# Kernel tuning notes

Hardware: AMD Instinct MI355X
Metric: run time of the kernel (lower is better)

## Reference

```python
import jax, jax.numpy as jnp
import numpy as np

B, V, D = 8, 201, 256          # batch episodes, nodes (way*shot+1), feature dim
H = 128                        # hidden_dim
CHANS = [D, 2 * H, 2 * H, H, H]  # channel widths per ratio [2,2,1,1]
K = int(0.5 * V)               # beta * V = 100
EPS = 1e-5
SLOPE = 0.01                   # LeakyReLU default negative slope


def setup_inputs() -> dict:
    key = jax.random.key(0)
    ks = jax.random.split(key, 24)
    inp = {"x": jax.random.normal(ks[0], (B, V, D), dtype=jnp.float32)}
    j = 1
    for i in range(4):  # conv + BN blocks
        cin, cout = CHANS[i], CHANS[i + 1]
        inp[f"w{i}"] = jax.random.normal(ks[j], (cout, cin), dtype=jnp.float32) * (1.0 / np.sqrt(cin)); j += 1
        inp[f"b{i}"] = jax.random.normal(ks[j], (cout,), dtype=jnp.float32) * 0.02; j += 1
        inp[f"g{i}"] = 1.0 + 0.1 * jax.random.normal(ks[j], (cout,), dtype=jnp.float32); j += 1
        inp[f"be{i}"] = 0.1 * jax.random.normal(ks[j], (cout,), dtype=jnp.float32); j += 1
    inp["w4"] = jax.random.normal(ks[j], (1, CHANS[-1]), dtype=jnp.float32) * (1.0 / np.sqrt(CHANS[-1])); j += 1
    inp["b4"] = jax.random.normal(ks[j], (1,), dtype=jnp.float32) * 0.02
    return inp


def _bn(a, g, be):
    # BatchNorm2d training-mode forward: batch stats over (B, V, V) per channel
    m = a.mean(axis=(0, 1, 2))
    v = a.var(axis=(0, 1, 2))
    return (a - m) / jnp.sqrt(v + EPS) * g + be


def _block(a, w, b, g, be):
    # 1x1 conv == per-pixel GEMM in channel dim; layout [B,V,V,C]
    a = jnp.einsum("bvwc,oc->bvwo", a, w) + b
    a = _bn(a, g, be)
    return jnp.where(a >= 0, a, SLOPE * a)  # LeakyReLU


def reference(x, w0, b0, g0, be0, w1, b1, g1, be1, w2, b2, g2, be2,
              w3, b3, g3, be3, w4, b4):
    # pairwise abs-diff: [B, V, V, D]
    a = jnp.abs(x[:, :, None, :] - x[:, None, :, :])
    a = _block(a, w0, b0, g0, be0)
    a = _block(a, w1, b1, g1, be1)
    a = _block(a, w2, b2, g2, be2)
    a = _block(a, w3, b3, g3, be3)
    a = jnp.einsum("bvwc,oc->bvwo", a, w4) + b4   # [B, V, V, 1]
    A = jax.nn.softmax(a[..., 0], axis=2)         # softmax over second V axis
    # topk scatter mask, fully vectorized over batch and rows
    vals, idx = jax.lax.top_k(A, K)               # [B, V, K]
    bi = jnp.arange(B)[:, None, None]
    vi = jnp.arange(V)[None, :, None]
    mask_A = jnp.zeros_like(A).at[bi, vi, idx].set(vals)
    return mask_A
```

## Files before the change

### kernel.cpp

```cpp
#include <hip/hip_runtime.h>
#include <math.h>

#define NB 8
#define NV 201
#define ND 256
#define NPIX (NB*NV*NV)
#define TRI  (NV*(NV+1)/2)
#define NSYM (NB*TRI)
#define KSEL 100
#define BN_EPS 1e-5f
#define SLOPE 0.01f

__device__ __forceinline__ float lrelu(float v) { return v >= 0.f ? v : SLOPE * v; }

typedef _Float16 half4_t __attribute__((ext_vector_type(4)));
typedef _Float16 half8   __attribute__((ext_vector_type(8)));
typedef float    f32x4   __attribute__((ext_vector_type(4)));

__device__ __forceinline__ half4_t to_h4(float4 v) {
    half4_t h;
    h.x = (_Float16)v.x; h.y = (_Float16)v.y;
    h.z = (_Float16)v.z; h.w = (_Float16)v.w;
    return h;
}
__device__ __forceinline__ half4_t residual_h4(float4 v, half4_t h) {
    half4_t l;
    l.x = (_Float16)(v.x - (float)h.x); l.y = (_Float16)(v.y - (float)h.y);
    l.z = (_Float16)(v.z - (float)h.z); l.w = (_Float16)(v.w - (float)h.w);
    return l;
}
__device__ __forceinline__ half8 cat8(half4_t a, half4_t b) {
    half8 r;
    r[0] = a.x; r[1] = a.y; r[2] = a.z; r[3] = a.w;
    r[4] = b.x; r[5] = b.y; r[6] = b.z; r[7] = b.w;
    return r;
}

__device__ __forceinline__ int tri_base(int i) { return i * NV - (i * (i - 1)) / 2; }
__device__ __forceinline__ void tri_decode(int s, int& b, int& i, int& j) {
    b = s / TRI;
    int t = s - b * TRI;
    float disc = (float)(403 * 403) - 8.0f * (float)t;
    int ii = (int)((403.0f - sqrtf(disc)) * 0.5f);
    if (ii < 0) ii = 0;
    if (ii > NV - 1) ii = NV - 1;
    while (ii < NV - 1 && tri_base(ii + 1) <= t) ++ii;
    while (ii > 0 && tri_base(ii) > t) --ii;
    i = ii;
    j = t - tri_base(ii) + ii;
}

__device__ __forceinline__ float4 ld4(const float* p) { return *(const float4*)p; }

__global__ void zero_stats(double* p) { p[blockIdx.x * 256 + threadIdx.x] = 0.0; }

template<int CIN, int COUT, int MODE>
__global__ __launch_bounds__(256)
void gemm_bn_mfma(const float* xin,
                  const float* in,
                  const float* __restrict__ W,
                  const float* __restrict__ scale,
                  const float* __restrict__ shift,
                  float* out,
                  double* __restrict__ stat_sum,
                  double* __restrict__ stat_sq)
{
    constexpr int BM  = 128;
    constexpr int BK  = 32;
    constexpr int PAD = 40;
    constexpr int NCW = COUT / 32;
    __shared__ __align__(16) _Float16 Bh[COUT][PAD];
    __shared__ __align__(16) _Float16 Bl[COUT][PAD];
    __shared__ float wg[BM];
    __shared__ int   rbi[(MODE == 0) ? BM : 1];
    __shared__ int   rbj[(MODE == 0) ? BM : 1];

    const int t    = threadIdx.x;
    const int lane = t & 63;
    const int wv   = t >> 6;
    const int wm   = wv >> 1;
    const int wn   = wv & 1;
    const int l15  = lane & 15;
    const int lk   = lane >> 4;
    const int m0   = blockIdx.x * BM;

    for (int m = t; m < BM; m += 256) {
        int pix = m0 + m;
        int b, i, j;
        if (pix < NSYM) {
            tri_decode(pix, b, i, j);
            wg[m] = (i == j) ? 1.f : 2.f;
            if constexpr (MODE == 0) { rbi[m] = b * NV + i; rbj[m] = b * NV + j; }
        } else {
            wg[m] = 0.f;
            if constexpr (MODE == 0) { rbi[m] = 0; rbj[m] = 0; }
        }
    }

    f32x4 acc[4][NCW];
    #pragma unroll
    for (int rt = 0; rt < 4; ++rt)
        #pragma unroll
        for (int nc = 0; nc < NCW; ++nc) {
            acc[rt][nc][0] = 0.f; acc[rt][nc][1] = 0.f;
            acc[rt][nc][2] = 0.f; acc[rt][nc][3] = 0.f;
        }

    for (int kt = 0; kt < CIN; kt += BK) {
        #pragma unroll
        for (int f = 0; f < COUT / 32; ++f) {
            int flat = t + 256 * f;
            int n    = flat >> 3;
            int kq   = flat & 7;
            int k    = kt + kq * 4;
            float4 w = *(const float4*)(W + (size_t)n * CIN + k);
            half4_t vh = to_h4(w);
            half4_t vl = residual_h4(w, vh);
            *(half4_t*)&Bh[n][kq * 4] = vh;
            *(half4_t*)&Bl[n][kq * 4] = vl;
        }
        __syncthreads();

        float4 sc0, sc1, sh0, sh1;
        if constexpr (MODE == 1) {
            sc0 = ld4(scale + kt + lk * 8); sc1 = ld4(scale + kt + lk * 8 + 4);
            sh0 = ld4(shift + kt + lk * 8); sh1 = ld4(shift + kt + lk * 8 + 4);
        }
        half8 ah[4], alo[4];
        #pragma unroll
        for (int rt = 0; rt < 4; ++rt) {
            int m   = wm * 64 + rt * 16 + l15;
            int pix = m0 + m;
            float4 v0 = make_float4(0.f, 0.f, 0.f, 0.f);
            float4 v1 = v0;
            if (pix < NSYM) {
                if constexpr (MODE == 0) {
                    const float* pi = xin + (size_t)rbi[m] * ND + kt + lk * 8;
                    const float* pj = xin + (size_t)rbj[m] * ND + kt + lk * 8;
                    float4 xi0 = ld4(pi), xi1 = ld4(pi + 4);
                    float4 xj0 = ld4(pj), xj1 = ld4(pj + 4);
                    v0 = make_float4(fabsf(xi0.x - xj0.x), fabsf(xi0.y - xj0.y),
                                     fabsf(xi0.z - xj0.z), fabsf(xi0.w - xj0.w));
                    v1 = make_float4(fabsf(xi1.x - xj1.x), fabsf(xi1.y - xj1.y),
                                     fabsf(xi1.z - xj1.z), fabsf(xi1.w - xj1.w));
                } else {
                    const float* p = in + (size_t)pix * 256 + kt + lk * 8;
                    float4 u0 = ld4(p), u1 = ld4(p + 4);
                    v0.x = lrelu(fmaf(u0.x, sc0.x, sh0.x));
                    v0.y = lrelu(fmaf(u0.y, sc0.y, sh0.y));
                    v0.z = lrelu(fmaf(u0.z, sc0.z, sh0.z));
                    v0.w = lrelu(fmaf(u0.w, sc0.w, sh0.w));
                    v1.x = lrelu(fmaf(u1.x, sc1.x, sh1.x));
                    v1.y = lrelu(fmaf(u1.y, sc1.y, sh1.y));
                    v1.z = lrelu(fmaf(u1.z, sc1.z, sh1.z));
                    v1.w = lrelu(fmaf(u1.w, sc1.w, sh1.w));
                }
            }
            half4_t h0 = to_h4(v0), h1 = to_h4(v1);
            half4_t l0 = residual_h4(v0, h0), l1 = residual_h4(v1, h1);
            ah[rt]  = cat8(h0, h1);
            alo[rt] = cat8(l0, l1);
        }

        #pragma unroll
        for (int nc = 0; nc < NCW; ++nc) {
            int ctrow = (wn * NCW + nc) * 16 + l15;
            half8 bh = *(const half8*)&Bh[ctrow][lk * 8];
            half8 bl = *(const half8*)&Bl[ctrow][lk * 8];
            #pragma unroll
            for (int rt = 0; rt < 4; ++rt) {
                acc[rt][nc] = __builtin_amdgcn_mfma_f32_16x16x32_f16(ah[rt],  bh, acc[rt][nc], 0, 0, 0);
                acc[rt][nc] = __builtin_amdgcn_mfma_f32_16x16x32_f16(ah[rt],  bl, acc[rt][nc], 0, 0, 0);
                acc[rt][nc] = __builtin_amdgcn_mfma_f32_16x16x32_f16(alo[rt], bh, acc[rt][nc], 0, 0, 0);
            }
        }
        __syncthreads();
    }

    float* csum = (float*)&Bh[0][0];
    float* csq  = csum + COUT;
    for (int n = t; n < COUT; n += 256) { csum[n] = 0.f; csq[n] = 0.f; }
    __syncthreads();

    float tsum[NCW], tsq[NCW];
    #pragma unroll
    for (int nc = 0; nc < NCW; ++nc) { tsum[nc] = 0.f; tsq[nc] = 0.f; }

    #pragma unroll
    for (int rt = 0; rt < 4; ++rt) {
        #pragma unroll
        for (int r = 0; r < 4; ++r) {
            int row = wm * 64 + rt * 16 + lk * 4 + r;
            int pix = m0 + row;
            if (pix < NSYM) {
                float wgt = wg[row];
                #pragma unroll
                for (int nc = 0; nc < NCW; ++nc) {
                    float v = acc[rt][nc][r];
                    tsum[nc] += wgt * v;
                    tsq[nc]  += wgt * v * v;
                    out[(size_t)pix * 256 + wn * (COUT / 2) + nc * 16 + l15] = v;
                }
            }
        }
    }
    #pragma unroll
    for (int nc = 0; nc < NCW; ++nc) {
        int col = wn * (COUT / 2) + nc * 16 + l15;
        atomicAdd(&csum[col], tsum[nc]);
        atomicAdd(&csq[col],  tsq[nc]);
    }
    __syncthreads();
    for (int n = t; n < COUT; n += 256) {
        atomicAdd(&stat_sum[n], (double)csum[n]);
        atomicAdd(&stat_sq[n],  (double)csq[n]);
    }
}

__global__ void bn_finalize(const double* __restrict__ ssum, const double* __restrict__ ssq,
                            const float* __restrict__ g, const float* __restrict__ be,
                            float* __restrict__ scale, float* __restrict__ shift, int C)
{
    int c = threadIdx.x + blockIdx.x * blockDim.x;
    if (c < C) {
        double m = ssum[c] * (1.0 / NPIX);
        double v = ssq[c] * (1.0 / NPIX) - m * m;
        float s = g[c] / sqrtf((float)v + BN_EPS);
        scale[c] = s;
        shift[c] = be[c] - (float)m * s;
    }
}

__global__ __launch_bounds__(256)
void logits_tri(const float* __restrict__ act,
                const float* __restrict__ scale, const float* __restrict__ shift,
                const float* __restrict__ w4, const float* __restrict__ b4,
                float* __restrict__ lt)
{
    int s = blockIdx.x * 256 + threadIdx.x;
    if (s >= NSYM) return;
    const float* p = act + (size_t)s * 256;
    float acc = 0.f;
    #pragma unroll
    for (int c = 0; c < 128; c += 4) {
        float4 u  = ld4(p + c);
        float4 sc = *(const float4*)(scale + c);
        float4 sh = *(const float4*)(shift + c);
        float4 w  = *(const float4*)(w4 + c);
        acc += lrelu(fmaf(u.x, sc.x, sh.x)) * w.x;
        acc += lrelu(fmaf(u.y, sc.y, sh.y)) * w.y;
        acc += lrelu(fmaf(u.z, sc.z, sh.z)) * w.z;
        acc += lrelu(fmaf(u.w, sc.w, sh.w)) * w.w;
    }
    lt[s] = acc + b4[0];
}

__global__ __launch_bounds__(256)
void final_softmax_topk_sym(const float* __restrict__ lt, float* __restrict__ outp)
{
    __shared__ float sv[NV];
    __shared__ float red[256];
    const int row = blockIdx.x;
    const int b   = row / NV;
    const int i   = row - b * NV;
    const int t   = threadIdx.x;

    float logit = -INFINITY;
    if (t < NV) {
        int jm = (i < t) ? i : t;
        int jM = (i < t) ? t : i;
        logit = lt[b * TRI + tri_base(jm) + (jM - jm)];
    }
    red[t] = logit;
    __syncthreads();
    #pragma unroll
    for (int off = 128; off > 0; off >>= 1) {
        if (t < off) red[t] = fmaxf(red[t], red[t + off]);
        __syncthreads();
    }
    float mx = red[0];
    __syncthreads();
    float e = (t < NV) ? expf(logit - mx) : 0.f;
    red[t] = e;
    __syncthreads();
    #pragma unroll
    for (int off = 128; off > 0; off >>= 1) {
        if (t < off) red[t] += red[t + off];
        __syncthreads();
    }
    float denom = red[0];
    __syncthreads();
    float val = e / denom;
    if (t < NV) sv[t] = val;
    __syncthreads();
    if (t < NV) {
        int rank = 0;
        for (int j = 0; j < NV; ++j) {
            float o = sv[j];
            rank += (o > val || (o == val && j < t)) ? 1 : 0;
        }
        outp[(size_t)row * NV + t] = (rank < KSEL) ? val : 0.f;
    }
}

extern "C" void kernel_launch(void* const* d_in, const int* in_sizes, int n_in,
                              void* d_out, int out_size, void* d_ws, size_t ws_size,
                              hipStream_t stream)
{
    (void)in_sizes; (void)n_in; (void)out_size; (void)ws_size;

    const float* x   = (const float*)d_in[0];
    const float* w0  = (const float*)d_in[1];
    const float* g0  = (const float*)d_in[3];
    const float* be0 = (const float*)d_in[4];
    const float* w1  = (const float*)d_in[5];
    const float* g1  = (const float*)d_in[7];
    const float* be1 = (const float*)d_in[8];
    const float* w2  = (const float*)d_in[9];
    const float* g2  = (const float*)d_in[11];
    const float* be2 = (const float*)d_in[12];
    const float* w3  = (const float*)d_in[13];
    const float* g3  = (const float*)d_in[15];
    const float* be3 = (const float*)d_in[16];
    const float* w4  = (const float*)d_in[17];
    const float* b4  = (const float*)d_in[18];

    char* ws = (char*)d_ws;
    double* D    = (double*)ws;
    float*  F    = (float*)(ws + 16384);
    float*  lt   = (float*)(ws + 16384 + 8192);
    float*  buf  = (float*)(ws + 16384 + 8192 + 655360);
    float*  outp = (float*)d_out;

    zero_stats<<<8, 256, 0, stream>>>(D);

    const int g128 = (NSYM + 127) / 128;

    gemm_bn_mfma<256, 256, 0><<<g128, 256, 0, stream>>>(
        x, nullptr, w0, nullptr, nullptr, buf, D + 0, D + 256);
    bn_finalize<<<1, 256, 0, stream>>>(D + 0, D + 256, g0, be0, F + 0, F + 256, 256);

    gemm_bn_mfma<256, 256, 1><<<g128, 256, 0, stream>>>(
        nullptr, buf, w1, F + 0, F + 256, buf, D + 512, D + 768);
    bn_finalize<<<1, 256, 0, stream>>>(D + 512, D + 768, g1, be1, F + 512, F + 768, 256);

    gemm_bn_mfma<256, 128, 1><<<g128, 256, 0, stream>>>(
        nullptr, buf, w2, F + 512, F + 768, buf, D + 1024, D + 1280);
    bn_finalize<<<1, 256, 0, stream>>>(D + 1024, D + 1280, g2, be2, F + 1024, F + 1280, 128);

    gemm_bn_mfma<128, 128, 1><<<g128, 256, 0, stream>>>(
        nullptr, buf, w3, F + 1024, F + 1280, buf, D + 1536, D + 1792);
    bn_finalize<<<1, 256, 0, stream>>>(D + 1536, D + 1792, g3, be3, F + 1536, F + 1792, 128);

    logits_tri<<<(NSYM + 255) / 256, 256, 0, stream>>>(buf, F + 1536, F + 1792, w4, b4, lt);
    final_softmax_topk_sym<<<NB * NV, 256, 0, stream>>>(lt, outp);
}
```

Measured before the change: 664.9 us.

## Pre-split weights to fp16 hi/lo once and read B fragments directly from global

Adds a one-time kernel that splits all four conv weight matrices into fp16 high and low residual parts, stored in the output buffer as scratch. The GEMM kernels then load B fragments straight from global or L2 instead of converting and staging weights through shared memory every K-tile. This removes the per-tile conversion work and two barriers per K iteration. In exchange, each wave now issues uncoalesced-ish global loads for weights, and the output buffer is reused as temporary storage before the final kernel overwrites it.

```diff
diff --git a/kernel.cpp b/kernel.cpp
--- a/kernel.cpp
+++ b/kernel.cpp
@@ -10,6 +10,7 @@
 #define KSEL 100
 #define BN_EPS 1e-5f
 #define SLOPE 0.01f
+#define NWTOT 180224
 
 __device__ __forceinline__ float lrelu(float v) { return v >= 0.f ? v : SLOPE * v; }
 
@@ -54,11 +55,28 @@
 
 __global__ void zero_stats(double* p) { p[blockIdx.x * 256 + threadIdx.x] = 0.0; }
 
+__global__ void split_weights(const float* __restrict__ w0, const float* __restrict__ w1,
+                              const float* __restrict__ w2, const float* __restrict__ w3,
+                              _Float16* __restrict__ H, _Float16* __restrict__ L)
+{
+    int idx = blockIdx.x * 256 + threadIdx.x;
+    if (idx >= NWTOT) return;
+    float v;
+    if      (idx <  65536) v = w0[idx];
+    else if (idx < 131072) v = w1[idx -  65536];
+    else if (idx < 163840) v = w2[idx - 131072];
+    else                   v = w3[idx - 163840];
+    _Float16 h = (_Float16)v;
+    H[idx] = h;
+    L[idx] = (_Float16)(v - (float)h);
+}
+
 template<int CIN, int COUT, int MODE>
 __global__ __launch_bounds__(256)
 void gemm_bn_mfma(const float* xin,
                   const float* in,
-                  const float* __restrict__ W,
+                  const _Float16* __restrict__ Wh,
+                  const _Float16* __restrict__ Wl,
                   const float* __restrict__ scale,
                   const float* __restrict__ shift,
                   float* out,
@@ -67,13 +85,12 @@
 {
     constexpr int BM  = 128;
     constexpr int BK  = 32;
-    constexpr int PAD = 40;
     constexpr int NCW = COUT / 32;
-    __shared__ __align__(16) _Float16 Bh[COUT][PAD];
-    __shared__ __align__(16) _Float16 Bl[COUT][PAD];
     __shared__ float wg[BM];
     __shared__ int   rbi[(MODE == 0) ? BM : 1];
     __shared__ int   rbj[(MODE == 0) ? BM : 1];
+    __shared__ float csum[COUT];
+    __shared__ float csq[COUT];
 
     const int t    = threadIdx.x;
     const int lane = t & 63;
@@ -96,6 +113,7 @@
             if constexpr (MODE == 0) { rbi[m] = 0; rbj[m] = 0; }
         }
     }
+    __syncthreads();
 
     f32x4 acc[4][NCW];
     #pragma unroll
@@ -107,20 +125,6 @@
         }
 
     for (int kt = 0; kt < CIN; kt += BK) {
-        #pragma unroll
-        for (int f = 0; f < COUT / 32; ++f) {
-            int flat = t + 256 * f;
-            int n    = flat >> 3;
-            int kq   = flat & 7;
-            int k    = kt + kq * 4;
-            float4 w = *(const float4*)(W + (size_t)n * CIN + k);
-            half4_t vh = to_h4(w);
-            half4_t vl = residual_h4(w, vh);
-            *(half4_t*)&Bh[n][kq * 4] = vh;
-            *(half4_t*)&Bl[n][kq * 4] = vl;
-        }
-        __syncthreads();
-
         float4 sc0, sc1, sh0, sh1;
         if constexpr (MODE == 1) {
             sc0 = ld4(scale + kt + lk * 8); sc1 = ld4(scale + kt + lk * 8 + 4);
@@ -164,9 +168,9 @@
 
         #pragma unroll
         for (int nc = 0; nc < NCW; ++nc) {
-            int ctrow = (wn * NCW + nc) * 16 + l15;
-            half8 bh = *(const half8*)&Bh[ctrow][lk * 8];
-            half8 bl = *(const half8*)&Bl[ctrow][lk * 8];
+            size_t boff = (size_t)(wn * (COUT / 2) + nc * 16 + l15) * CIN + kt + lk * 8;
+            half8 bh = *(const half8*)(Wh + boff);
+            half8 bl = *(const half8*)(Wl + boff);
             #pragma unroll
             for (int rt = 0; rt < 4; ++rt) {
                 acc[rt][nc] = __builtin_amdgcn_mfma_f32_16x16x32_f16(ah[rt],  bh, acc[rt][nc], 0, 0, 0);
@@ -174,11 +178,8 @@
                 acc[rt][nc] = __builtin_amdgcn_mfma_f32_16x16x32_f16(alo[rt], bh, acc[rt][nc], 0, 0, 0);
             }
         }
-        __syncthreads();
-    }
-
-    float* csum = (float*)&Bh[0][0];
-    float* csq  = csum + COUT;
+    }
+
     for (int n = t; n < COUT; n += 256) { csum[n] = 0.f; csq[n] = 0.f; }
     __syncthreads();
 
@@ -332,24 +333,28 @@
     float*  buf  = (float*)(ws + 16384 + 8192 + 655360);
     float*  outp = (float*)d_out;
 
+    _Float16* WH = (_Float16*)d_out;
+    _Float16* WL = WH + NWTOT;
+
     zero_stats<<<8, 256, 0, stream>>>(D);
+    split_weights<<<(NWTOT + 255) / 256, 256, 0, stream>>>(w0, w1, w2, w3, WH, WL);
 
     const int g128 = (NSYM + 127) / 128;
 
     gemm_bn_mfma<256, 256, 0><<<g128, 256, 0, stream>>>(
-        x, nullptr, w0, nullptr, nullptr, buf, D + 0, D + 256);
+        x, nullptr, WH + 0, WL + 0, nullptr, nullptr, buf, D + 0, D + 256);
     bn_finalize<<<1, 256, 0, stream>>>(D + 0, D + 256, g0, be0, F + 0, F + 256, 256);
 
     gemm_bn_mfma<256, 256, 1><<<g128, 256, 0, stream>>>(
-        nullptr, buf, w1, F + 0, F + 256, buf, D + 512, D + 768);
+        nullptr, buf, WH + 65536, WL + 65536, F + 0, F + 256, buf, D + 512, D + 768);
     bn_finalize<<<1, 256, 0, stream>>>(D + 512, D + 768, g1, be1, F + 512, F + 768, 256);
 
     gemm_bn_mfma<256, 128, 1><<<g128, 256, 0, stream>>>(
-        nullptr, buf, w2, F + 512, F + 768, buf, D + 1024, D + 1280);
+        nullptr, buf, WH + 131072, WL + 131072, F + 512, F + 768, buf, D + 1024, D + 1280);
     bn_finalize<<<1, 256, 0, stream>>>(D + 1024, D + 1280, g2, be2, F + 1024, F + 1280, 128);
 
     gemm_bn_mfma<128, 128, 1><<<g128, 256, 0, stream>>>(
-        nullptr, buf, w3, F + 1024, F + 1280, buf, D + 1536, D + 1792);
+        nullptr, buf, WH + 163840, WL + 163840, F + 1024, F + 1280, buf, D + 1536, D + 1792);
     bn_finalize<<<1, 256, 0, stream>>>(D + 1536, D + 1792, g3, be3, F + 1536, F + 1792, 128);
 
     logits_tri<<<(NSYM + 255) / 256, 256, 0, stream>>>(buf, F + 1536, F + 1792, w4, b4, lt);
```

Result: slower. 739.7 us (+11.2%).
